# Kernel tuning notes

Hardware: AMD Instinct MI355X
Metric: run time of the kernel (lower is better)

## Reference

```python
import jax, jax.numpy as jnp
import numpy as np

T_LEN = 1024
N_IN = 512
BATCH = 32
SURR_ALPHA = 4.0  # slope of the sigmoid surrogate gradient


@jax.custom_vjp
def heaviside_sg(x):
    # spike = Heaviside(x); backward uses sigmoid surrogate derivative
    return (x >= 0).astype(x.dtype)

def _hs_fwd(x):
    return heaviside_sg(x), x

def _hs_bwd(x, g):
    s = jax.nn.sigmoid(SURR_ALPHA * x)
    return (g * SURR_ALPHA * s * (1.0 - s),)

heaviside_sg.defvjp(_hs_fwd, _hs_bwd)


def setup_inputs() -> dict:
    key = jax.random.key(0)
    k1, k2, k3 = jax.random.split(key, 3)
    current = jax.random.normal(k1, (T_LEN, BATCH, N_IN), dtype=jnp.float32)
    beta = jax.random.uniform(k2, (N_IN,), dtype=jnp.float32)  # per-channel decay in (0,1)
    v_init = jax.random.normal(k3, (BATCH, N_IN), dtype=jnp.float32)
    v_th = jnp.ones((T_LEN, BATCH, N_IN), dtype=jnp.float32)
    return {"current": current, "beta": beta, "v_init": v_init, "v_th": v_th}


def reference(current, beta, v_init, v_th):
    # Torch version: grouped causal conv1d with kernel beta^{T-1-k}, i.e.
    # membrane[t] = sum_{j<=t} beta^{t-j} * current[j], with current[0] += beta*v_init.
    # Equivalent O(T) linear recurrence: m_t = beta*m_{t-1} + c_t, m_{-1}=v_init.
    def step(m, c):
        m = beta * m + c  # beta (N,) broadcasts over (B,N)
        return m, m

    m_last, membrane = jax.lax.scan(step, v_init, current)  # membrane: (T,B,N)

    # surrogate-gradient spike function
    spikes = heaviside_sg(membrane - v_th)  # (T,B,N)

    # triangular phi kernel: z[t] = sum_{j<=t} (t-j+1)*spikes[j] == double cumsum
    z = jnp.cumsum(jnp.cumsum(spikes, axis=0), axis=0)  # (T,B,N)

    # Block.g: keep entries equal to 1, zero everything else; gradient is identity
    # (the subtracted term is detached in the torch code).
    gz = z - jax.lax.stop_gradient(jnp.where(z == 1.0, 0.0, z))

    return gz, z, m_last  # m_last == membrane[:, :, -1] in torch layout (B,N)
```

## Files before the change

kernel.cpp:

```cpp
#include <hip/hip_runtime.h>


#define T_LEN 1024
#define N_IN  512
#define BN    16384
#define U     16
#define DW    (T_LEN / 32)

struct Buf { float c[U]; float v[U]; };

__device__ __forceinline__ void prefetch(Buf& b, const float* __restrict__ cp,
                                         const float* __restrict__ vp, int t0) {
    if (t0 >= T_LEN) return;
    const float* __restrict__ c = cp + (size_t)t0 * BN;
    const float* __restrict__ v = vp + (size_t)t0 * BN;
#pragma unroll
    for (int u = 0; u < U; ++u) {
        b.c[u] = c[(size_t)u * BN];
        b.v[u] = v[(size_t)u * BN];
    }
}

__device__ __forceinline__ unsigned process16(const Buf& b, float beta, float& m,
                                              int& C, int& Z) {
    unsigned mask = 0u;
#pragma unroll
    for (int u = 0; u < U; ++u) {
        m = fmaf(beta, m, b.c[u]);
        const int s = (m >= b.v[u]) ? 1 : 0;
        mask |= (unsigned)s << u;
        C += s;
        Z += C;
    }
    return mask;
}


__global__ __launch_bounds__(64, 1) void snn_scan(
        const float* __restrict__ cur, const float* __restrict__ beta,
        const float* __restrict__ vini, const float* __restrict__ vth,
        unsigned* __restrict__ bitsg, unsigned* __restrict__ Pc,
        float* __restrict__ ml)
{
    const int i = blockIdx.x * 64 + threadIdx.x;
    const float bta = beta[i & (N_IN - 1)];
    float m = vini[i];
    int C = 0, Z = 0;

    const float* cp = cur + i;
    const float* vp = vth + i;

    Buf b0, b1, b2, b3;
    prefetch(b0, cp, vp, 0);
    prefetch(b1, cp, vp, U);
    prefetch(b2, cp, vp, 2 * U);
    prefetch(b3, cp, vp, 3 * U);

    for (int t0 = 0; t0 < T_LEN; t0 += 4 * U) {
        const int d = t0 >> 5;
        Pc[(size_t)d * BN + i] = (unsigned)C | ((unsigned)Z << 11);
        unsigned ma = process16(b0, bta, m, C, Z);   prefetch(b0, cp, vp, t0 + 4 * U);
        unsigned mb = process16(b1, bta, m, C, Z);   prefetch(b1, cp, vp, t0 + 5 * U);
        bitsg[(size_t)d * BN + i] = ma | (mb << 16);
        Pc[(size_t)(d + 1) * BN + i] = (unsigned)C | ((unsigned)Z << 11);
        ma = process16(b2, bta, m, C, Z);            prefetch(b2, cp, vp, t0 + 6 * U);
        mb = process16(b3, bta, m, C, Z);            prefetch(b3, cp, vp, t0 + 7 * U);
        bitsg[(size_t)(d + 1) * BN + i] = ma | (mb << 16);
    }
    ml[i] = m;
}

__global__ __launch_bounds__(256, 4) void snn_expand(
        const unsigned* __restrict__ bitsg, const unsigned* __restrict__ Pc,
        float* __restrict__ gz, float* __restrict__ zo)
{
    const int d  = blockIdx.x & (DW - 1);
    const int cb = blockIdx.x / DW;
    const int cg = threadIdx.x & 63;
    const int tt = threadIdx.x >> 6;
    const int ch = cb * 256 + cg * 4;

    const uint4 u  = *reinterpret_cast<const uint4*>(&bitsg[(size_t)d * BN + ch]);
    const uint4 p4 = *reinterpret_cast<const uint4*>(&Pc[(size_t)d * BN + ch]);
    int C0 = (int)(p4.x & 0x7FFu), Z0 = (int)(p4.x >> 11);
    int C1 = (int)(p4.y & 0x7FFu), Z1 = (int)(p4.y >> 11);
    int C2 = (int)(p4.z & 0x7FFu), Z2 = (int)(p4.z >> 11);
    int C3 = (int)(p4.w & 0x7FFu), Z3 = (int)(p4.w >> 11);

    const int pre = tt * 8;
    for (int b = 0; b < pre; ++b) {
        C0 += (int)((u.x >> b) & 1u); Z0 += C0;
        C1 += (int)((u.y >> b) & 1u); Z1 += C1;
        C2 += (int)((u.z >> b) & 1u); Z2 += C2;
        C3 += (int)((u.w >> b) & 1u); Z3 += C3;
    }

    float* __restrict__ gp = gz + (size_t)(d * 32 + pre) * BN + ch;
    float* __restrict__ zp = zo + (size_t)(d * 32 + pre) * BN + ch;
#pragma unroll
    for (int r = 0; r < 8; ++r) {
        const int b = pre + r;
        C0 += (int)((u.x >> b) & 1u); Z0 += C0;
        C1 += (int)((u.y >> b) & 1u); Z1 += C1;
        C2 += (int)((u.z >> b) & 1u); Z2 += C2;
        C3 += (int)((u.w >> b) & 1u); Z3 += C3;
        const float4 gf = make_float4(Z0 == 1 ? 1.0f : 0.0f,
                                      Z1 == 1 ? 1.0f : 0.0f,
                                      Z2 == 1 ? 1.0f : 0.0f,
                                      Z3 == 1 ? 1.0f : 0.0f);
        const float4 zf = make_float4((float)Z0, (float)Z1,
                                      (float)Z2, (float)Z3);
        *reinterpret_cast<float4*>(gp + (size_t)r * BN) = gf;
        *reinterpret_cast<float4*>(zp + (size_t)r * BN) = zf;
    }
}


__global__ __launch_bounds__(512, 2) void snn_fused(
        const float* __restrict__ cur, const float* __restrict__ beta,
        const float* __restrict__ vini, const float* __restrict__ vth,
        float* __restrict__ gz, float* __restrict__ zo, float* __restrict__ ml)
{
    __shared__ unsigned bits[T_LEN / 32][64];

    const int lane = threadIdx.x & 63;
    const int wave = threadIdx.x >> 6;
    const int i = blockIdx.x * 64 + lane;

    if (wave == 0) {
        const float bta = beta[i & (N_IN - 1)];
        float m = vini[i];
        int Cd = 0, Zd = 0;
        const float* cp = cur + i;
        const float* vp = vth + i;

        Buf b0, b1, b2, b3;
        prefetch(b0, cp, vp, 0);
        prefetch(b1, cp, vp, U);
        prefetch(b2, cp, vp, 2 * U);
        prefetch(b3, cp, vp, 3 * U);

        for (int t0 = 0; t0 < T_LEN; t0 += 4 * U) {
            unsigned m0 = process16(b0, bta, m, Cd, Zd);
            prefetch(b0, cp, vp, t0 + 4 * U);
            unsigned m1 = process16(b1, bta, m, Cd, Zd);
            prefetch(b1, cp, vp, t0 + 5 * U);
            bits[t0 >> 5][lane] = m0 | (m1 << 16);
            unsigned m2 = process16(b2, bta, m, Cd, Zd);
            prefetch(b2, cp, vp, t0 + 6 * U);
            unsigned m3 = process16(b3, bta, m, Cd, Zd);
            prefetch(b3, cp, vp, t0 + 7 * U);
            bits[(t0 >> 5) + 1][lane] = m2 | (m3 << 16);
        }
        ml[i] = m;
    }
    __syncthreads();

    int C = 0, Z = 0;
    const int d0 = wave * 4;
    for (int d = 0; d < d0; ++d) {
        unsigned u = bits[d][lane];
#pragma unroll
        for (int b = 0; b < 32; ++b) { C += (u >> b) & 1u; Z += C; }
    }

    float* __restrict__ gp = gz + (size_t)(d0 * 32) * BN + i;
    float* __restrict__ zp = zo + (size_t)(d0 * 32) * BN + i;
    for (int d = 0; d < 4; ++d) {
        unsigned u = bits[d0 + d][lane];
#pragma unroll
        for (int b = 0; b < 32; ++b) {
            C += (u >> b) & 1u;
            Z += C;
            const size_t off = (size_t)(d * 32 + b) * BN;
            gp[off] = (Z == 1) ? 1.0f : 0.0f;
            zp[off] = (float)Z;
        }
    }
}

extern "C" void kernel_launch(void* const* d_in, const int* in_sizes, int n_in,
                              void* d_out, int out_size, void* d_ws, size_t ws_size,
                              hipStream_t stream) {
    const float* cur  = (const float*)d_in[0];
    const float* beta = (const float*)d_in[1];
    const float* vini = (const float*)d_in[2];
    const float* vth  = (const float*)d_in[3];
    float* gz = (float*)d_out;
    float* zo = gz + (size_t)T_LEN * BN;
    float* ml = zo + (size_t)T_LEN * BN;

    const size_t need = (size_t)DW * BN * sizeof(unsigned) * 2;

    if (d_ws != nullptr && ws_size >= need) {
        unsigned* bitsg = (unsigned*)d_ws;
        unsigned* Pc = bitsg + (size_t)DW * BN;
        snn_scan<<<BN / 64, 64, 0, stream>>>(cur, beta, vini, vth, bitsg, Pc, ml);
        snn_expand<<<DW * (BN / 256), 256, 0, stream>>>(bitsg, Pc, gz, zo);
    } else {
        snn_fused<<<BN / 64, 512, 0, stream>>>(cur, beta, vini, vth, gz, zo, ml);
    }
}
```

Baseline: 252.9 us.

## Stage scan inputs through double-buffered LDS via producer waves and async loads

The scan kernel now uses 192-thread blocks, with two producer waves issuing global_load_lds copies of current and threshold segments of 64 time steps into double-buffered shared memory. A single consumer wave runs the serial recurrence reading from LDS. Block barriers separate the segments. The goal is to hide global memory latency on the latency-bound serial scan, replacing the register prefetch scheme. The costs are 64KB of LDS per block and a barrier per segment. The fallback fused kernel also drops its unused C/Z counters.

```diff
diff --git a/kernel.cpp b/kernel.cpp
--- a/kernel.cpp
+++ b/kernel.cpp
@@ -6,68 +6,81 @@
 #define BN    16384
 #define U     16
 #define DW    (T_LEN / 32)
-
-struct Buf { float c[U]; float v[U]; };
-
-__device__ __forceinline__ void prefetch(Buf& b, const float* __restrict__ cp,
-                                         const float* __restrict__ vp, int t0) {
-    if (t0 >= T_LEN) return;
-    const float* __restrict__ c = cp + (size_t)t0 * BN;
-    const float* __restrict__ v = vp + (size_t)t0 * BN;
-#pragma unroll
-    for (int u = 0; u < U; ++u) {
-        b.c[u] = c[(size_t)u * BN];
-        b.v[u] = v[(size_t)u * BN];
-    }
-}
-
-__device__ __forceinline__ unsigned process16(const Buf& b, float beta, float& m,
-                                              int& C, int& Z) {
-    unsigned mask = 0u;
-#pragma unroll
-    for (int u = 0; u < U; ++u) {
-        m = fmaf(beta, m, b.c[u]);
-        const int s = (m >= b.v[u]) ? 1 : 0;
-        mask |= (unsigned)s << u;
-        C += s;
-        Z += C;
-    }
-    return mask;
-}
-
-
-__global__ __launch_bounds__(64, 1) void snn_scan(
+#define SEG_T 64
+#define NSEG  (T_LEN / SEG_T)
+
+__device__ __forceinline__ void gload_lds16(const float* g, float* l) {
+    __builtin_amdgcn_global_load_lds(
+        (const __attribute__((address_space(1))) void*)g,
+        (__attribute__((address_space(3))) void*)l, 16, 0, 0);
+}
+
+__device__ __forceinline__ void issue_seg(const float* __restrict__ src,
+                                          float* dst, int s, size_t goff) {
+#pragma unroll
+    for (int j = 0; j < SEG_T / 4; ++j) {
+        gload_lds16(src + (size_t)(SEG_T * s + 4 * j) * BN + goff, dst + j * 256);
+    }
+}
+
+
+__global__ __launch_bounds__(192, 1) void snn_scan(
         const float* __restrict__ cur, const float* __restrict__ beta,
         const float* __restrict__ vini, const float* __restrict__ vth,
         unsigned* __restrict__ bitsg, unsigned* __restrict__ Pc,
         float* __restrict__ ml)
 {
-    const int i = blockIdx.x * 64 + threadIdx.x;
-    const float bta = beta[i & (N_IN - 1)];
-    float m = vini[i];
+    __shared__ float ldsC[2][SEG_T * 64];
+    __shared__ float ldsV[2][SEG_T * 64];
+
+    const int lane   = threadIdx.x & 63;
+    const int wave   = threadIdx.x >> 6;
+    const int chbase = blockIdx.x * 64;
+    const size_t goff = (size_t)chbase + (size_t)(lane >> 4) * BN
+                      + (size_t)(4 * (lane & 15));
+
+    float bta = 0.0f, m = 0.0f;
     int C = 0, Z = 0;
-
-    const float* cp = cur + i;
-    const float* vp = vth + i;
-
-    Buf b0, b1, b2, b3;
-    prefetch(b0, cp, vp, 0);
-    prefetch(b1, cp, vp, U);
-    prefetch(b2, cp, vp, 2 * U);
-    prefetch(b3, cp, vp, 3 * U);
-
-    for (int t0 = 0; t0 < T_LEN; t0 += 4 * U) {
-        const int d = t0 >> 5;
-        Pc[(size_t)d * BN + i] = (unsigned)C | ((unsigned)Z << 11);
-        unsigned ma = process16(b0, bta, m, C, Z);   prefetch(b0, cp, vp, t0 + 4 * U);
-        unsigned mb = process16(b1, bta, m, C, Z);   prefetch(b1, cp, vp, t0 + 5 * U);
-        bitsg[(size_t)d * BN + i] = ma | (mb << 16);
-        Pc[(size_t)(d + 1) * BN + i] = (unsigned)C | ((unsigned)Z << 11);
-        ma = process16(b2, bta, m, C, Z);            prefetch(b2, cp, vp, t0 + 6 * U);
-        mb = process16(b3, bta, m, C, Z);            prefetch(b3, cp, vp, t0 + 7 * U);
-        bitsg[(size_t)(d + 1) * BN + i] = ma | (mb << 16);
-    }
-    ml[i] = m;
+    if (wave == 0) {
+        bta = beta[(chbase + lane) & (N_IN - 1)];
+        m   = vini[chbase + lane];
+    }
+
+    if (wave == 1) issue_seg(cur, &ldsC[0][0], 0, goff);
+    if (wave == 2) issue_seg(vth, &ldsV[0][0], 0, goff);
+    __syncthreads();
+
+    for (int s = 0; s < NSEG; ++s) {
+        const int cb = s & 1, nb = (s + 1) & 1;
+        if (s + 1 < NSEG) {
+            if (wave == 1) issue_seg(cur, &ldsC[nb][0], s + 1, goff);
+            if (wave == 2) issue_seg(vth, &ldsV[nb][0], s + 1, goff);
+        }
+        if (wave == 0) {
+            const float* lc = &ldsC[cb][lane];
+            const float* lv = &ldsV[cb][lane];
+            const int i = chbase + lane;
+#pragma unroll
+            for (int h = 0; h < SEG_T / 32; ++h) {
+                const int d = s * (SEG_T / 32) + h;
+                Pc[(size_t)d * BN + i] = (unsigned)C | ((unsigned)Z << 11);
+                unsigned mask = 0u;
+#pragma unroll
+                for (int t = 0; t < 32; ++t) {
+                    const float c = lc[(h * 32 + t) * 64];
+                    const float v = lv[(h * 32 + t) * 64];
+                    m = fmaf(bta, m, c);
+                    const int sp = (m >= v) ? 1 : 0;
+                    mask |= (unsigned)sp << t;
+                    C += sp;
+                    Z += C;
+                }
+                bitsg[(size_t)d * BN + i] = mask;
+            }
+        }
+        __syncthreads();
+    }
+    if (wave == 0) ml[chbase + lane] = m;
 }
 
 __global__ __launch_bounds__(256, 4) void snn_expand(
@@ -116,6 +129,30 @@
 }
 
 
+struct Buf { float c[U]; float v[U]; };
+
+__device__ __forceinline__ void prefetch(Buf& b, const float* __restrict__ cp,
+                                         const float* __restrict__ vp, int t0) {
+    if (t0 >= T_LEN) return;
+    const float* __restrict__ c = cp + (size_t)t0 * BN;
+    const float* __restrict__ v = vp + (size_t)t0 * BN;
+#pragma unroll
+    for (int u = 0; u < U; ++u) {
+        b.c[u] = c[(size_t)u * BN];
+        b.v[u] = v[(size_t)u * BN];
+    }
+}
+
+__device__ __forceinline__ unsigned process16(const Buf& b, float beta, float& m) {
+    unsigned mask = 0u;
+#pragma unroll
+    for (int u = 0; u < U; ++u) {
+        m = fmaf(beta, m, b.c[u]);
+        mask |= (m >= b.v[u]) ? (1u << u) : 0u;
+    }
+    return mask;
+}
+
 __global__ __launch_bounds__(512, 2) void snn_fused(
         const float* __restrict__ cur, const float* __restrict__ beta,
         const float* __restrict__ vini, const float* __restrict__ vth,
@@ -130,7 +167,6 @@
     if (wave == 0) {
         const float bta = beta[i & (N_IN - 1)];
         float m = vini[i];
-        int Cd = 0, Zd = 0;
         const float* cp = cur + i;
         const float* vp = vth + i;
 
@@ -141,14 +177,14 @@
         prefetch(b3, cp, vp, 3 * U);
 
         for (int t0 = 0; t0 < T_LEN; t0 += 4 * U) {
-            unsigned m0 = process16(b0, bta, m, Cd, Zd);
+            unsigned m0 = process16(b0, bta, m);
             prefetch(b0, cp, vp, t0 + 4 * U);
-            unsigned m1 = process16(b1, bta, m, Cd, Zd);
+            unsigned m1 = process16(b1, bta, m);
             prefetch(b1, cp, vp, t0 + 5 * U);
             bits[t0 >> 5][lane] = m0 | (m1 << 16);
-            unsigned m2 = process16(b2, bta, m, Cd, Zd);
+            unsigned m2 = process16(b2, bta, m);
             prefetch(b2, cp, vp, t0 + 6 * U);
-            unsigned m3 = process16(b3, bta, m, Cd, Zd);
+            unsigned m3 = process16(b3, bta, m);
             prefetch(b3, cp, vp, t0 + 7 * U);
             bits[(t0 >> 5) + 1][lane] = m2 | (m3 << 16);
         }
@@ -195,7 +231,7 @@
     if (d_ws != nullptr && ws_size >= need) {
         unsigned* bitsg = (unsigned*)d_ws;
         unsigned* Pc = bitsg + (size_t)DW * BN;
-        snn_scan<<<BN / 64, 64, 0, stream>>>(cur, beta, vini, vth, bitsg, Pc, ml);
+        snn_scan<<<BN / 64, 192, 0, stream>>>(cur, beta, vini, vth, bitsg, Pc, ml);
         snn_expand<<<DW * (BN / 256), 256, 0, stream>>>(bitsg, Pc, gz, zo);
     } else {
         snn_fused<<<BN / 64, 512, 0, stream>>>(cur, beta, vini, vth, gz, zo, ml);
```

Result: faster. 244.4 us (-3.4%).

## Use warp-specialized producer/consumer scan with LDS ring buffer and float4 loads

Applied to the files above, without the earlier changes.

Replaces the per-thread strided scan kernel with a 768-thread block in which four producer waves load current and threshold tiles as float4 into a padded shared-memory ring buffer. Four consumer waves run the recurrence from LDS, and the two groups coordinate through volatile flag spinning. The aim is wider coalesced global loads and more memory-level parallelism than one 64-thread wave per block with a register prefetch. The cost is much larger LDS use (about 139 KB per block), only 64 blocks on the GPU, and spin-wait synchronization overhead. It also relies on volatile LDS ordering for correctness.

```diff
diff --git a/kernel.cpp b/kernel.cpp
--- a/kernel.cpp
+++ b/kernel.cpp
@@ -4,70 +4,110 @@
 #define T_LEN 1024
 #define N_IN  512
 #define BN    16384
-#define U     16
 #define DW    (T_LEN / 32)
 
-struct Buf { float c[U]; float v[U]; };
-
-__device__ __forceinline__ void prefetch(Buf& b, const float* __restrict__ cp,
-                                         const float* __restrict__ vp, int t0) {
-    if (t0 >= T_LEN) return;
-    const float* __restrict__ c = cp + (size_t)t0 * BN;
-    const float* __restrict__ v = vp + (size_t)t0 * BN;
-#pragma unroll
-    for (int u = 0; u < U; ++u) {
-        b.c[u] = c[(size_t)u * BN];
-        b.v[u] = v[(size_t)u * BN];
-    }
-}
-
-__device__ __forceinline__ unsigned process16(const Buf& b, float beta, float& m,
-                                              int& C, int& Z) {
-    unsigned mask = 0u;
-#pragma unroll
-    for (int u = 0; u < U; ++u) {
-        m = fmaf(beta, m, b.c[u]);
-        const int s = (m >= b.v[u]) ? 1 : 0;
-        mask |= (unsigned)s << u;
-        C += s;
-        Z += C;
-    }
-    return mask;
-}
-
-
-__global__ __launch_bounds__(64, 1) void snn_scan(
+#define CHB   256
+#define NBLK1 (BN / CHB)
+#define SEGT  16
+#define NSEG1 (T_LEN / SEGT)
+#define RING1 4
+#define TPAD  17
+
+__global__ __launch_bounds__(768, 1) void snn_scan_wide(
         const float* __restrict__ cur, const float* __restrict__ beta,
         const float* __restrict__ vini, const float* __restrict__ vth,
         unsigned* __restrict__ bitsg, unsigned* __restrict__ Pc,
         float* __restrict__ ml)
 {
-    const int i = blockIdx.x * 64 + threadIdx.x;
-    const float bta = beta[i & (N_IN - 1)];
-    float m = vini[i];
-    int C = 0, Z = 0;
-
-    const float* cp = cur + i;
-    const float* vp = vth + i;
-
-    Buf b0, b1, b2, b3;
-    prefetch(b0, cp, vp, 0);
-    prefetch(b1, cp, vp, U);
-    prefetch(b2, cp, vp, 2 * U);
-    prefetch(b3, cp, vp, 3 * U);
-
-    for (int t0 = 0; t0 < T_LEN; t0 += 4 * U) {
-        const int d = t0 >> 5;
-        Pc[(size_t)d * BN + i] = (unsigned)C | ((unsigned)Z << 11);
-        unsigned ma = process16(b0, bta, m, C, Z);   prefetch(b0, cp, vp, t0 + 4 * U);
-        unsigned mb = process16(b1, bta, m, C, Z);   prefetch(b1, cp, vp, t0 + 5 * U);
-        bitsg[(size_t)d * BN + i] = ma | (mb << 16);
-        Pc[(size_t)(d + 1) * BN + i] = (unsigned)C | ((unsigned)Z << 11);
-        ma = process16(b2, bta, m, C, Z);            prefetch(b2, cp, vp, t0 + 6 * U);
-        mb = process16(b3, bta, m, C, Z);            prefetch(b3, cp, vp, t0 + 7 * U);
-        bitsg[(size_t)(d + 1) * BN + i] = ma | (mb << 16);
-    }
-    ml[i] = m;
+    __shared__ float stage[2 * RING1 * CHB * TPAD];
+    __shared__ volatile int prod[2][RING1];
+    __shared__ volatile int scons[4];
+
+    const int lane   = threadIdx.x & 63;
+    const int wave   = threadIdx.x >> 6;
+    const int chbase = blockIdx.x * CHB;
+
+    if (threadIdx.x < 8)  prod[threadIdx.x & 1][threadIdx.x >> 1] = 0;
+    if (threadIdx.x < 4)  scons[threadIdx.x] = 0;
+    __syncthreads();
+
+    if (wave >= 4) {
+        const int w = wave - 4;
+        const int a = w & 1;
+        const int r = w >> 1;
+        const float* __restrict__ src = (a == 0) ? cur : vth;
+
+        for (int s = r; s < NSEG1; s += RING1) {
+            if (s >= RING1) {
+                const int need = s - RING1 + 1;
+                while (scons[0] < need || scons[1] < need ||
+                       scons[2] < need || scons[3] < need)
+                    __builtin_amdgcn_s_sleep(1);
+                asm volatile("" ::: "memory");
+            }
+            float4 rg[SEGT];
+#pragma unroll
+            for (int t = 0; t < SEGT; ++t)
+                rg[t] = *reinterpret_cast<const float4*>(
+                            src + (size_t)(s * SEGT + t) * BN + chbase + 4 * lane);
+            float* base = &stage[((a * RING1 + (s & (RING1 - 1))) * CHB
+                                  + 4 * lane) * TPAD];
+#pragma unroll
+            for (int t = 0; t < SEGT; ++t) {
+                base[0 * TPAD + t] = rg[t].x;
+                base[1 * TPAD + t] = rg[t].y;
+                base[2 * TPAD + t] = rg[t].z;
+                base[3 * TPAD + t] = rg[t].w;
+            }
+            asm volatile("s_waitcnt lgkmcnt(0)" ::: "memory");
+            prod[a][s & (RING1 - 1)] = s + 1;
+        }
+    } else {
+        const int i = chbase + 64 * wave + lane;
+        const int chl = 64 * wave + lane;
+        const float bta = beta[i & (N_IN - 1)];
+        float m = vini[i];
+        int C = 0, Z = 0;
+        unsigned mlo = 0u;
+
+        const float* cbase = &stage[(0 * RING1 * CHB + chl) * TPAD];
+        const float* vbase = &stage[(1 * RING1 * CHB + chl) * TPAD];
+
+#pragma unroll 1
+        for (int s = 0; s < NSEG1; ++s) {
+            const int sl = s & (RING1 - 1);
+            while (prod[0][sl] < s + 1 || prod[1][sl] < s + 1)
+                __builtin_amdgcn_s_sleep(1);
+            asm volatile("" ::: "memory");
+
+            if ((s & 1) == 0)
+                Pc[(size_t)(s >> 1) * BN + i] = (unsigned)C | ((unsigned)Z << 11);
+
+            const float* lc = cbase + sl * CHB * TPAD;
+            const float* lv = vbase + sl * CHB * TPAD;
+            float cc[SEGT], vv[SEGT];
+#pragma unroll
+            for (int t = 0; t < SEGT; ++t) { cc[t] = lc[t]; vv[t] = lv[t]; }
+
+            unsigned mask = 0u;
+#pragma unroll
+            for (int t = 0; t < SEGT; ++t) {
+                m = fmaf(bta, m, cc[t]);
+                const int sp = (m >= vv[t]) ? 1 : 0;
+                mask |= (unsigned)sp << t;
+                C += sp;
+                Z += C;
+            }
+            if ((s & 1) == 0) {
+                mlo = mask;
+            } else {
+                bitsg[(size_t)(s >> 1) * BN + i] = mlo | (mask << 16);
+            }
+            asm volatile("s_waitcnt lgkmcnt(0)" ::: "memory");
+            if (lane == 0) scons[wave] = s + 1;
+        }
+        ml[i] = m;
+    }
 }
 
 __global__ __launch_bounds__(256, 4) void snn_expand(
@@ -115,14 +155,37 @@
     }
 }
 
-
-__global__ __launch_bounds__(512, 2) void snn_fused(
+#define U 16
+struct Buf { float c[U]; float v[U]; };
+
+__device__ __forceinline__ void prefetch(Buf& b, const float* __restrict__ cp,
+                                         const float* __restrict__ vp, int t0) {
+    if (t0 >= T_LEN) return;
+    const float* __restrict__ c = cp + (size_t)t0 * BN;
+    const float* __restrict__ v = vp + (size_t)t0 * BN;
+#pragma unroll
+    for (int u = 0; u < U; ++u) {
+        b.c[u] = c[(size_t)u * BN];
+        b.v[u] = v[(size_t)u * BN];
+    }
+}
+
+__device__ __forceinline__ unsigned process16(const Buf& b, float beta, float& m) {
+    unsigned mask = 0u;
+#pragma unroll
+    for (int u = 0; u < U; ++u) {
+        m = fmaf(beta, m, b.c[u]);
+        mask |= (m >= b.v[u]) ? (1u << u) : 0u;
+    }
+    return mask;
+}
+
+__global__ __launch_bounds__(512, 2) void snn_fused_fb(
         const float* __restrict__ cur, const float* __restrict__ beta,
         const float* __restrict__ vini, const float* __restrict__ vth,
         float* __restrict__ gz, float* __restrict__ zo, float* __restrict__ ml)
 {
     __shared__ unsigned bits[T_LEN / 32][64];
-
     const int lane = threadIdx.x & 63;
     const int wave = threadIdx.x >> 6;
     const int i = blockIdx.x * 64 + lane;
@@ -130,26 +193,17 @@
     if (wave == 0) {
         const float bta = beta[i & (N_IN - 1)];
         float m = vini[i];
-        int Cd = 0, Zd = 0;
         const float* cp = cur + i;
         const float* vp = vth + i;
-
         Buf b0, b1, b2, b3;
-        prefetch(b0, cp, vp, 0);
-        prefetch(b1, cp, vp, U);
-        prefetch(b2, cp, vp, 2 * U);
-        prefetch(b3, cp, vp, 3 * U);
-
+        prefetch(b0, cp, vp, 0);     prefetch(b1, cp, vp, U);
+        prefetch(b2, cp, vp, 2 * U); prefetch(b3, cp, vp, 3 * U);
         for (int t0 = 0; t0 < T_LEN; t0 += 4 * U) {
-            unsigned m0 = process16(b0, bta, m, Cd, Zd);
-            prefetch(b0, cp, vp, t0 + 4 * U);
-            unsigned m1 = process16(b1, bta, m, Cd, Zd);
-            prefetch(b1, cp, vp, t0 + 5 * U);
+            unsigned m0 = process16(b0, bta, m); prefetch(b0, cp, vp, t0 + 4 * U);
+            unsigned m1 = process16(b1, bta, m); prefetch(b1, cp, vp, t0 + 5 * U);
             bits[t0 >> 5][lane] = m0 | (m1 << 16);
-            unsigned m2 = process16(b2, bta, m, Cd, Zd);
-            prefetch(b2, cp, vp, t0 + 6 * U);
-            unsigned m3 = process16(b3, bta, m, Cd, Zd);
-            prefetch(b3, cp, vp, t0 + 7 * U);
+            unsigned m2 = process16(b2, bta, m); prefetch(b2, cp, vp, t0 + 6 * U);
+            unsigned m3 = process16(b3, bta, m); prefetch(b3, cp, vp, t0 + 7 * U);
             bits[(t0 >> 5) + 1][lane] = m2 | (m3 << 16);
         }
         ml[i] = m;
@@ -163,7 +217,6 @@
 #pragma unroll
         for (int b = 0; b < 32; ++b) { C += (u >> b) & 1u; Z += C; }
     }
-
     float* __restrict__ gp = gz + (size_t)(d0 * 32) * BN + i;
     float* __restrict__ zp = zo + (size_t)(d0 * 32) * BN + i;
     for (int d = 0; d < 4; ++d) {
@@ -195,9 +248,11 @@
     if (d_ws != nullptr && ws_size >= need) {
         unsigned* bitsg = (unsigned*)d_ws;
         unsigned* Pc = bitsg + (size_t)DW * BN;
-        snn_scan<<<BN / 64, 64, 0, stream>>>(cur, beta, vini, vth, bitsg, Pc, ml);
+        snn_scan_wide<<<NBLK1, 768, 0, stream>>>(cur, beta, vini, vth,
+                                                 bitsg, Pc, ml);
         snn_expand<<<DW * (BN / 256), 256, 0, stream>>>(bitsg, Pc, gz, zo);
     } else {
-        snn_fused<<<BN / 64, 512, 0, stream>>>(cur, beta, vini, vth, gz, zo, ml);
-    }
-}
+        snn_fused_fb<<<BN / 64, 512, 0, stream>>>(cur, beta, vini, vth,
+                                                  gz, zo, ml);
+    }
+}
```

After: 267.3 us. 1.06x slower.
